# Kernel tuning notes

Hardware: AMD Instinct MI355X
Metric: run time of the kernel (lower is better)

Reference implementation:

```python
import jax, jax.numpy as jnp
import numpy as np

INPUT_DIM = 512
OUTPUT_DIM = 512
DEGREE = 7
ALPHA = 0.5


def setup_inputs() -> dict:
    key = jax.random.key(0)
    kx, kc = jax.random.split(key)
    x = jax.random.normal(kx, (8192, INPUT_DIM), dtype=jnp.float32)
    std = 1.0 / (INPUT_DIM * (DEGREE + 1))
    laguerre_coeffs = jax.random.normal(kc, (INPUT_DIM, OUTPUT_DIM, DEGREE + 1), dtype=jnp.float32) * std
    return {"x": x, "laguerre_coeffs": laguerre_coeffs}


def reference(x, laguerre_coeffs):
    # x: [B, I] -> tanh squashed
    xt = jnp.tanh(x.reshape(-1, INPUT_DIM))
    # Build Laguerre basis L_0..L_degree via the standard recurrence:
    # k*L_k = (2(k-1)+1+alpha - x)*L_{k-1} - (k-1+alpha)*L_{k-2}
    L0 = jnp.ones_like(xt)
    basis = [L0]
    if DEGREE > 0:
        L1 = 1.0 + ALPHA - xt
        basis.append(L1)
        Lkm2, Lkm1 = L0, L1
        for k in range(2, DEGREE + 1):
            Lk = ((2 * (k - 1) + 1 + ALPHA - xt) * Lkm1 - (k - 1 + ALPHA) * Lkm2) / k
            basis.append(Lk)
            Lkm2, Lkm1 = Lkm1, Lk
    laguerre = jnp.stack(basis, axis=-1)  # [B, I, D+1]
    y = jnp.einsum('bid,iod->bo', laguerre, laguerre_coeffs)
    return y
```

## Files before the change

kernel.cpp:

```cpp
#include <hip/hip_runtime.h>

#define B_ROWS 8192
#define IN_DIM 512
#define OUT_DIM 512
#define NDEG 8
#define KDIM (IN_DIM * NDEG)
#define ZSLICES 4
#define NKT 16
#define BM 256
#define BN 128
#define LDB 72

typedef short bf16x8 __attribute__((ext_vector_type(8)));
typedef float f32x4  __attribute__((ext_vector_type(4)));

__device__ __forceinline__ unsigned short f2bf(float f) {
  unsigned u = __float_as_uint(f);
  u += 0x7fffu + ((u >> 16) & 1u);
  return (unsigned short)(u >> 16);
}

__device__ __forceinline__ void laguerre8(float t, float* L) {
  L[0] = 1.0f;
  L[1] = 1.5f - t;
#pragma unroll
  for (int k = 2; k < NDEG; ++k)
    L[k] = ((2.0f * (float)k - 0.5f - t) * L[k - 1] -
            ((float)k - 0.5f) * L[k - 2]) * (1.0f / (float)k);
  }

__global__ void prep_kernel(const float* __restrict__ x, const float* __restrict__ cf,
                            unsigned short* __restrict__ A, unsigned short* __restrict__ Bt) {
  int g = blockIdx.x;
  if (g < (B_ROWS * IN_DIM) / 256) {
    int idx = g * 256 + threadIdx.x;
    int b = idx >> 9, i = idx & 511;
    float L[NDEG];
    laguerre8(tanhf(x[idx]), L);
    uint4 v;
    v.x = (unsigned)f2bf(L[0]) | ((unsigned)f2bf(L[1]) << 16);
    v.y = (unsigned)f2bf(L[2]) | ((unsigned)f2bf(L[3]) << 16);
    v.z = (unsigned)f2bf(L[4]) | ((unsigned)f2bf(L[5]) << 16);
    v.w = (unsigned)f2bf(L[6]) | ((unsigned)f2bf(L[7]) << 16);
    int T = b >> 8, r = b & 255, kt = i >> 3, c = i & 7;
    size_t chunk = ((size_t)(T * 64 + kt)) * 2048 + r * 8 + (c ^ (r & 7));
    ((uint4*)A)[chunk] = v;
  } else {
    int idx = (g - (B_ROWS * IN_DIM) / 256) * 256 + threadIdx.x;
    int i = idx >> 9, o = idx & 511;
    const float4* cp = (const float4*)(cf + (size_t)idx * 8);
    float4 c0 = cp[0], c1 = cp[1];
    uint4 v;
    v.x = (unsigned)f2bf(c0.x) | ((unsigned)f2bf(c0.y) << 16);
    v.y = (unsigned)f2bf(c0.z) | ((unsigned)f2bf(c0.w) << 16);
    v.z = (unsigned)f2bf(c1.x) | ((unsigned)f2bf(c1.y) << 16);
    v.w = (unsigned)f2bf(c1.z) | ((unsigned)f2bf(c1.w) << 16);
    ((uint4*)Bt)[o * 512 + i] = v;
  }
}

__global__ __launch_bounds__(512, 2) void gemm_kernel(const unsigned short* __restrict__ A,
                                                      const unsigned short* __restrict__ Bt,
                                                      unsigned short* __restrict__ P) {
  __shared__ unsigned short lds[51200];

  const int tid = threadIdx.x;
  const int lane = tid & 63;
  const int w = tid >> 6;
  const int wm = w >> 1, wn = w & 1;

  const int g = blockIdx.x;
  const int xcd = g & 7, idx = g >> 3;
  const int z = xcd >> 1;
  const int y = (xcd & 1) * 16 + (idx & 15);
  const int bn = (idx >> 4) * BN;

  const uint4* Ag = (const uint4*)A;
  const uint4* Bg = (const uint4*)Bt;
  const size_t tile0 = ((size_t)(y * 64 + z * NKT)) * 2048;

  const int rB = tid >> 2, cB = (tid & 3) * 2;

  const int arow = lane & 15, hi = lane >> 4;
  const int swz0 = hi ^ (arow & 7);
  const int aoff0 = (wm * 64 + arow) * 64 + swz0 * 8;
  const int aoff1 = (wm * 64 + arow) * 64 + (swz0 ^ 4) * 8;
  const int boff  = (wn * 64 + arow) * LDB;

  f32x4 zero = {0.f, 0.f, 0.f, 0.f};
  f32x4 acc[4][4];
#pragma unroll
  for (int mi = 0; mi < 4; ++mi)
#pragma unroll
    for (int ni = 0; ni < 4; ++ni) acc[mi][ni] = zero;

  uint4 rb0 = Bg[(size_t)(bn + rB) * 512 + z * NKT * 8 + cB];
  uint4 rb1 = Bg[(size_t)(bn + rB) * 512 + z * NKT * 8 + cB + 1];
  {
    size_t base = tile0 + w * 256;
    unsigned short* dst = lds + w * 2048;
#pragma unroll
    for (int j = 0; j < 4; ++j)
      __builtin_amdgcn_global_load_lds(
          (const __attribute__((address_space(1))) unsigned int*)(Ag + base + j * 64 + lane),
          (__attribute__((address_space(3))) unsigned int*)(dst + j * 512), 16, 0, 0);
  }
  *(uint4*)&lds[32768 + rB * LDB + cB * 8] = rb0;
  *(uint4*)&lds[32768 + rB * LDB + (cB + 1) * 8] = rb1;
  __syncthreads();

#pragma unroll 2
  for (int kt = 0; kt < NKT; ++kt) {
    const int cur = kt & 1, nb = cur ^ 1;
    if (kt + 1 < NKT) {
      rb0 = Bg[(size_t)(bn + rB) * 512 + (z * NKT + kt + 1) * 8 + cB];
      rb1 = Bg[(size_t)(bn + rB) * 512 + (z * NKT + kt + 1) * 8 + cB + 1];
      size_t base = tile0 + (size_t)(kt + 1) * 2048 + w * 256;
      unsigned short* dst = lds + nb * 16384 + w * 2048;
#pragma unroll
      for (int j = 0; j < 4; ++j)
        __builtin_amdgcn_global_load_lds(
            (const __attribute__((address_space(1))) unsigned int*)(Ag + base + (size_t)(kt + 1) * 0 + base - base + j * 64 + lane),
            (__attribute__((address_space(3))) unsigned int*)(dst + j * 512), 16, 0, 0);
      __builtin_amdgcn_sched_barrier(0);
    }

    const unsigned short* Ac = lds + cur * 16384;
    const unsigned short* Bc = lds + 32768 + cur * 9216;
    bf16x8 af0[4], af1[4], bf0[4], bf1[4];
#pragma unroll
    for (int mi = 0; mi < 4; ++mi) {
      af0[mi] = *(const bf16x8*)(Ac + aoff0 + mi * 1024);
      af1[mi] = *(const bf16x8*)(Ac + aoff1 + mi * 1024);
    }
#pragma unroll
    for (int ni = 0; ni < 4; ++ni) {
      bf0[ni] = *(const bf16x8*)(Bc + boff + ni * 16 * LDB + hi * 8);
      bf1[ni] = *(const bf16x8*)(Bc + boff + ni * 16 * LDB + 32 + hi * 8);
    }
    __builtin_amdgcn_s_setprio(1);
#pragma unroll
    for (int mi = 0; mi < 4; ++mi)
#pragma unroll
      for (int ni = 0; ni < 4; ++ni)
        acc[mi][ni] = __builtin_amdgcn_mfma_f32_16x16x32_bf16(af0[mi], bf0[ni], acc[mi][ni], 0, 0, 0);
#pragma unroll
    for (int mi = 0; mi < 4; ++mi)
#pragma unroll
      for (int ni = 0; ni < 4; ++ni)
        acc[mi][ni] = __builtin_amdgcn_mfma_f32_16x16x32_bf16(af1[mi], bf1[ni], acc[mi][ni], 0, 0, 0);
    __builtin_amdgcn_s_setprio(0);

    if (kt + 1 < NKT) {
      unsigned short* BsN = lds + 32768 + nb * 9216;
      *(uint4*)&BsN[rB * LDB + cB * 8] = rb0;
      *(uint4*)&BsN[rB * LDB + (cB + 1) * 8] = rb1;
    }
    __syncthreads();
  }

  unsigned short* W = lds + w * 4096;
#pragma unroll
  for (int mi = 0; mi < 4; ++mi)
#pragma unroll
    for (int ni = 0; ni < 4; ++ni) {
      int col = ni * 16 + arow;
      int c8 = col >> 3, cpos = col & 7;
#pragma unroll
      for (int r = 0; r < 4; ++r) {
        int row = mi * 16 + hi * 4 + r;
        W[row * 64 + ((c8 ^ (row & 7)) << 3) + cpos] = f2bf(acc[mi][ni][r]);
      }
    }
  const int rr = lane >> 3, cc = lane & 7;
#pragma unroll
  for (int it = 0; it < 8; ++it) {
    int row = it * 8 + rr;
    uint4 v = *(uint4*)&W[row * 64 + ((cc ^ (row & 7)) << 3)];
    size_t pr = ((size_t)z * B_ROWS + (y * 256 + wm * 64 + row)) * 512 + bn + wn * 64 + cc * 8;
    *(uint4*)&P[pr] = v;
  }
}

__global__ void reduce_kernel(const unsigned short* __restrict__ P, float* __restrict__ out) {
  size_t t = (size_t)blockIdx.x * 256 + threadIdx.x;
  const uint4* p = (const uint4*)P;
  const size_t stride = (size_t)B_ROWS * OUT_DIM / 8;
  float s[8] = {0, 0, 0, 0, 0, 0, 0, 0};
#pragma unroll
  for (int zz = 0; zz < ZSLICES; ++zz) {
    uint4 v = p[t + zz * stride];
    unsigned q[4] = {v.x, v.y, v.z, v.w};
#pragma unroll
    for (int j = 0; j < 4; ++j) {
      s[2 * j]     += __uint_as_float((q[j] & 0xffffu) << 16);
      s[2 * j + 1] += __uint_as_float(q[j] & 0xffff0000u);
    }
  }
  float4 o0 = {s[0], s[1], s[2], s[3]}, o1 = {s[4], s[5], s[6], s[7]};
  ((float4*)out)[t * 2]     = o0;
  ((float4*)out)[t * 2 + 1] = o1;
}

__global__ void naive_kernel(const float* __restrict__ x, const float* __restrict__ c,
                             float* __restrict__ out) {
  __shared__ float bas[IN_DIM * NDEG];
  int b = blockIdx.x;
  for (int i = threadIdx.x; i < IN_DIM; i += 256) {
    float t = tanhf(x[(size_t)b * IN_DIM + i]);
    float L[NDEG];
    laguerre8(t, L);
#pragma unroll
    for (int d = 0; d < NDEG; ++d) bas[i * NDEG + d] = L[d];
  }
  __syncthreads();
  for (int o = threadIdx.x; o < OUT_DIM; o += 256) {
    float acc = 0.f;
    for (int i = 0; i < IN_DIM; ++i) {
      const float* cp = c + ((size_t)i * OUT_DIM + o) * NDEG;
#pragma unroll
      for (int d = 0; d < NDEG; ++d) acc += bas[i * NDEG + d] * cp[d];
    }
    out[(size_t)b * OUT_DIM + o] = acc;
  }
}

extern "C" void kernel_launch(void* const* d_in, const int* in_sizes, int n_in,
                              void* d_out, int out_size, void* d_ws, size_t ws_size,
                              hipStream_t stream) {
  const float* x    = (const float*)d_in[0];
  const float* coef = (const float*)d_in[1];
  float* out = (float*)d_out;

  const size_t A_BYTES  = (size_t)B_ROWS * KDIM * 2;
  const size_t P_BYTES  = (size_t)ZSLICES * B_ROWS * OUT_DIM * 2;
  const size_t BT_BYTES = (size_t)OUT_DIM * KDIM * 2;

  if (ws_size >= A_BYTES + P_BYTES + BT_BYTES) {
    unsigned short* Abuf = (unsigned short*)d_ws;
    unsigned short* Pp   = (unsigned short*)((char*)d_ws + A_BYTES);
    unsigned short* Bt   = (unsigned short*)((char*)d_ws + A_BYTES + P_BYTES);
    prep_kernel<<<(B_ROWS * IN_DIM + IN_DIM * OUT_DIM) / 256, 256, 0, stream>>>(x, coef, Abuf, Bt);
    gemm_kernel<<<512, 512, 0, stream>>>(Abuf, Bt, Pp);
    reduce_kernel<<<(B_ROWS * OUT_DIM / 8) / 256, 256, 0, stream>>>(Pp, out);
  } else {
    naive_kernel<<<B_ROWS, 256, 0, stream>>>(x, coef, out);
  }
}
```

Measured before the change: 75.14 us.

## Enlarge GEMM tile to 256x256 with swizzled B layout and async LDS loads

```diff
diff --git a/kernel.cpp b/kernel.cpp
--- a/kernel.cpp
+++ b/kernel.cpp
@@ -7,9 +7,6 @@
 #define KDIM (IN_DIM * NDEG)
 #define ZSLICES 4
 #define NKT 16
-#define BM 256
-#define BN 128
-#define LDB 72
 
 typedef short bf16x8 __attribute__((ext_vector_type(8)));
 typedef float f32x4  __attribute__((ext_vector_type(4)));
@@ -27,7 +24,8 @@
   for (int k = 2; k < NDEG; ++k)
     L[k] = ((2.0f * (float)k - 0.5f - t) * L[k - 1] -
             ((float)k - 0.5f) * L[k - 2]) * (1.0f / (float)k);
-  }
+}
+
 
 __global__ void prep_kernel(const float* __restrict__ x, const float* __restrict__ cf,
                             unsigned short* __restrict__ A, unsigned short* __restrict__ Bt) {
@@ -42,8 +40,8 @@
     v.y = (unsigned)f2bf(L[2]) | ((unsigned)f2bf(L[3]) << 16);
     v.z = (unsigned)f2bf(L[4]) | ((unsigned)f2bf(L[5]) << 16);
     v.w = (unsigned)f2bf(L[6]) | ((unsigned)f2bf(L[7]) << 16);
-    int T = b >> 8, r = b & 255, kt = i >> 3, c = i & 7;
-    size_t chunk = ((size_t)(T * 64 + kt)) * 2048 + r * 8 + (c ^ (r & 7));
+    int h = b >> 7, rb = b & 127, t = i >> 3, c = i & 7;
+    size_t chunk = ((size_t)(h * 64 + t)) * 1024 + (rb >> 6) * 512 + (rb & 63) * 8 + (c ^ (rb & 7));
     ((uint4*)A)[chunk] = v;
   } else {
     int idx = (g - (B_ROWS * IN_DIM) / 256) * 256 + threadIdx.x;
@@ -55,113 +53,115 @@
     v.y = (unsigned)f2bf(c0.z) | ((unsigned)f2bf(c0.w) << 16);
     v.z = (unsigned)f2bf(c1.x) | ((unsigned)f2bf(c1.y) << 16);
     v.w = (unsigned)f2bf(c1.z) | ((unsigned)f2bf(c1.w) << 16);
-    ((uint4*)Bt)[o * 512 + i] = v;
+    int h = o >> 7, rb = o & 127, t = i >> 3, c = i & 7;
+    size_t chunk = ((size_t)(h * 64 + t)) * 1024 + (rb >> 6) * 512 + (rb & 63) * 8 + (c ^ (rb & 7));
+    ((uint4*)Bt)[chunk] = v;
   }
 }
 
 __global__ __launch_bounds__(512, 2) void gemm_kernel(const unsigned short* __restrict__ A,
                                                       const unsigned short* __restrict__ Bt,
                                                       unsigned short* __restrict__ P) {
-  __shared__ unsigned short lds[51200];
+  __shared__ unsigned short lds[65536];
 
   const int tid = threadIdx.x;
   const int lane = tid & 63;
   const int w = tid >> 6;
-  const int wm = w >> 1, wn = w & 1;
+  const int wm = w >> 2, wn = w & 3;
 
   const int g = blockIdx.x;
-  const int xcd = g & 7, idx = g >> 3;
-  const int z = xcd >> 1;
-  const int y = (xcd & 1) * 16 + (idx & 15);
-  const int bn = (idx >> 4) * BN;
+  const int j0 = g >> 3, xx = g & 7;
+  const int My = ((j0 >> 3) << 3) | xx;
+  const int n = (j0 >> 2) & 1;
+  const int z = j0 & 3;
 
   const uint4* Ag = (const uint4*)A;
   const uint4* Bg = (const uint4*)Bt;
-  const size_t tile0 = ((size_t)(y * 64 + z * NKT)) * 2048;
-
-  const int rB = tid >> 2, cB = (tid & 3) * 2;
 
   const int arow = lane & 15, hi = lane >> 4;
-  const int swz0 = hi ^ (arow & 7);
-  const int aoff0 = (wm * 64 + arow) * 64 + swz0 * 8;
-  const int aoff1 = (wm * 64 + arow) * 64 + (swz0 ^ 4) * 8;
-  const int boff  = (wn * 64 + arow) * LDB;
+  const int e0 = (hi ^ (arow & 7)) * 8;
 
   f32x4 zero = {0.f, 0.f, 0.f, 0.f};
-  f32x4 acc[4][4];
-#pragma unroll
-  for (int mi = 0; mi < 4; ++mi)
+  f32x4 acc[8][4];
+#pragma unroll
+  for (int mi = 0; mi < 8; ++mi)
 #pragma unroll
     for (int ni = 0; ni < 4; ++ni) acc[mi][ni] = zero;
 
-  uint4 rb0 = Bg[(size_t)(bn + rB) * 512 + z * NKT * 8 + cB];
-  uint4 rb1 = Bg[(size_t)(bn + rB) * 512 + z * NKT * 8 + cB + 1];
-  {
-    size_t base = tile0 + w * 256;
-    unsigned short* dst = lds + w * 2048;
-#pragma unroll
-    for (int j = 0; j < 4; ++j)
-      __builtin_amdgcn_global_load_lds(
-          (const __attribute__((address_space(1))) unsigned int*)(Ag + base + j * 64 + lane),
-          (__attribute__((address_space(3))) unsigned int*)(dst + j * 512), 16, 0, 0);
-  }
-  *(uint4*)&lds[32768 + rB * LDB + cB * 8] = rb0;
-  *(uint4*)&lds[32768 + rB * LDB + (cB + 1) * 8] = rb1;
+  auto STAGE = [&](int tile, int buf) {
+    const int tg = z * NKT + tile;
+    const size_t cA0 = ((size_t)((My * 2 + 0) * 64 + tg)) * 1024 + w * 64 + lane;
+    const size_t cA1 = ((size_t)((My * 2 + 1) * 64 + tg)) * 1024 + w * 64 + lane;
+    const size_t cB0 = ((size_t)((n * 2 + 0) * 64 + tg)) * 1024 + w * 64 + lane;
+    const size_t cB1 = ((size_t)((n * 2 + 1) * 64 + tg)) * 1024 + w * 64 + lane;
+    unsigned short* dA = lds + buf * 16384 + w * 512;
+    unsigned short* dB = lds + 32768 + buf * 16384 + w * 512;
+#pragma unroll
+    for (int j = 0; j < 2; ++j) {
+      __builtin_amdgcn_global_load_lds(
+          (const __attribute__((address_space(1))) unsigned int*)(Ag + cA0 + j * 512),
+          (__attribute__((address_space(3))) unsigned int*)(dA + j * 4096), 16, 0, 0);
+      __builtin_amdgcn_global_load_lds(
+          (const __attribute__((address_space(1))) unsigned int*)(Ag + cA1 + j * 512),
+          (__attribute__((address_space(3))) unsigned int*)(dA + 8192 + j * 4096), 16, 0, 0);
+      __builtin_amdgcn_global_load_lds(
+          (const __attribute__((address_space(1))) unsigned int*)(Bg + cB0 + j * 512),
+          (__attribute__((address_space(3))) unsigned int*)(dB + j * 4096), 16, 0, 0);
+      __builtin_amdgcn_global_load_lds(
+          (const __attribute__((address_space(1))) unsigned int*)(Bg + cB1 + j * 512),
+          (__attribute__((address_space(3))) unsigned int*)(dB + 8192 + j * 4096), 16, 0, 0);
+    }
+  };
+
+  auto COMPUTE = [&](int buf) {
+    const unsigned short* Ab = lds + buf * 16384 + wm * 8192;
+    const unsigned short* Bb = lds + 32768 + buf * 16384 + (wn >> 1) * 8192 + (wn & 1) * 4096;
+#pragma unroll
+    for (int ks = 0; ks < 2; ++ks) {
+      bf16x8 af[8], bfr[4];
+#pragma unroll
+      for (int mi = 0; mi < 8; ++mi)
+        af[mi] = *(const bf16x8*)(Ab + (mi >> 2) * 4096 + ((mi & 3) * 16 + arow) * 64 + (e0 ^ (ks * 32)));
+#pragma unroll
+      for (int ni = 0; ni < 4; ++ni)
+        bfr[ni] = *(const bf16x8*)(Bb + (ni * 16 + arow) * 64 + (e0 ^ (ks * 32)));
+      __builtin_amdgcn_s_setprio(1);
+#pragma unroll
+      for (int mi = 0; mi < 8; ++mi)
+#pragma unroll
+        for (int ni = 0; ni < 4; ++ni)
+          acc[mi][ni] = __builtin_amdgcn_mfma_f32_16x16x32_bf16(af[mi], bfr[ni], acc[mi][ni], 0, 0, 0);
+      __builtin_amdgcn_s_setprio(0);
+    }
+  };
+
+  STAGE(0, 0);
+  STAGE(1, 1);
+  asm volatile("s_waitcnt vmcnt(8)" ::: "memory");
+  __builtin_amdgcn_sched_barrier(0);
+  __builtin_amdgcn_s_barrier();
+
+  for (int t = 0; t < NKT - 2; ++t) {
+    const int cur = t & 1;
+    COMPUTE(cur);
+    asm volatile("s_waitcnt lgkmcnt(0)" ::: "memory");
+    __builtin_amdgcn_sched_barrier(0);
+    __builtin_amdgcn_s_barrier();
+    STAGE(t + 2, cur);
+    asm volatile("s_waitcnt vmcnt(8)" ::: "memory");
+    __builtin_amdgcn_sched_barrier(0);
+    __builtin_amdgcn_s_barrier();
+  }
+  COMPUTE(0);
+  asm volatile("s_waitcnt vmcnt(0)" ::: "memory");
+  __builtin_amdgcn_sched_barrier(0);
+  __builtin_amdgcn_s_barrier();
+  COMPUTE(1);
   __syncthreads();
 
-#pragma unroll 2
-  for (int kt = 0; kt < NKT; ++kt) {
-    const int cur = kt & 1, nb = cur ^ 1;
-    if (kt + 1 < NKT) {
-      rb0 = Bg[(size_t)(bn + rB) * 512 + (z * NKT + kt + 1) * 8 + cB];
-      rb1 = Bg[(size_t)(bn + rB) * 512 + (z * NKT + kt + 1) * 8 + cB + 1];
-      size_t base = tile0 + (size_t)(kt + 1) * 2048 + w * 256;
-      unsigned short* dst = lds + nb * 16384 + w * 2048;
-#pragma unroll
-      for (int j = 0; j < 4; ++j)
-        __builtin_amdgcn_global_load_lds(
-            (const __attribute__((address_space(1))) unsigned int*)(Ag + base + (size_t)(kt + 1) * 0 + base - base + j * 64 + lane),
-            (__attribute__((address_space(3))) unsigned int*)(dst + j * 512), 16, 0, 0);
-      __builtin_amdgcn_sched_barrier(0);
-    }
-
-    const unsigned short* Ac = lds + cur * 16384;
-    const unsigned short* Bc = lds + 32768 + cur * 9216;
-    bf16x8 af0[4], af1[4], bf0[4], bf1[4];
-#pragma unroll
-    for (int mi = 0; mi < 4; ++mi) {
-      af0[mi] = *(const bf16x8*)(Ac + aoff0 + mi * 1024);
-      af1[mi] = *(const bf16x8*)(Ac + aoff1 + mi * 1024);
-    }
-#pragma unroll
-    for (int ni = 0; ni < 4; ++ni) {
-      bf0[ni] = *(const bf16x8*)(Bc + boff + ni * 16 * LDB + hi * 8);
-      bf1[ni] = *(const bf16x8*)(Bc + boff + ni * 16 * LDB + 32 + hi * 8);
-    }
-    __builtin_amdgcn_s_setprio(1);
-#pragma unroll
-    for (int mi = 0; mi < 4; ++mi)
-#pragma unroll
-      for (int ni = 0; ni < 4; ++ni)
-        acc[mi][ni] = __builtin_amdgcn_mfma_f32_16x16x32_bf16(af0[mi], bf0[ni], acc[mi][ni], 0, 0, 0);
-#pragma unroll
-    for (int mi = 0; mi < 4; ++mi)
-#pragma unroll
-      for (int ni = 0; ni < 4; ++ni)
-        acc[mi][ni] = __builtin_amdgcn_mfma_f32_16x16x32_bf16(af1[mi], bf1[ni], acc[mi][ni], 0, 0, 0);
-    __builtin_amdgcn_s_setprio(0);
-
-    if (kt + 1 < NKT) {
-      unsigned short* BsN = lds + 32768 + nb * 9216;
-      *(uint4*)&BsN[rB * LDB + cB * 8] = rb0;
-      *(uint4*)&BsN[rB * LDB + (cB + 1) * 8] = rb1;
-    }
-    __syncthreads();
-  }
-
-  unsigned short* W = lds + w * 4096;
-#pragma unroll
-  for (int mi = 0; mi < 4; ++mi)
+  unsigned short* W = lds + w * 8192;
+#pragma unroll
+  for (int mi = 0; mi < 8; ++mi)
 #pragma unroll
     for (int ni = 0; ni < 4; ++ni) {
       int col = ni * 16 + arow;
@@ -174,10 +174,10 @@
     }
   const int rr = lane >> 3, cc = lane & 7;
 #pragma unroll
-  for (int it = 0; it < 8; ++it) {
+  for (int it = 0; it < 16; ++it) {
     int row = it * 8 + rr;
     uint4 v = *(uint4*)&W[row * 64 + ((cc ^ (row & 7)) << 3)];
-    size_t pr = ((size_t)z * B_ROWS + (y * 256 + wm * 64 + row)) * 512 + bn + wn * 64 + cc * 8;
+    size_t pr = ((size_t)z * B_ROWS + My * 256 + wm * 128 + row) * 512 + n * 256 + wn * 64 + cc * 8;
     *(uint4*)&P[pr] = v;
   }
 }
@@ -241,7 +241,7 @@
     unsigned short* Pp   = (unsigned short*)((char*)d_ws + A_BYTES);
     unsigned short* Bt   = (unsigned short*)((char*)d_ws + A_BYTES + P_BYTES);
     prep_kernel<<<(B_ROWS * IN_DIM + IN_DIM * OUT_DIM) / 256, 256, 0, stream>>>(x, coef, Abuf, Bt);
-    gemm_kernel<<<512, 512, 0, stream>>>(Abuf, Bt, Pp);
+    gemm_kernel<<<256, 512, 0, stream>>>(Abuf, Bt, Pp);
     reduce_kernel<<<(B_ROWS * OUT_DIM / 8) / 256, 256, 0, stream>>>(Pp, out);
   } else {
     naive_kernel<<<B_ROWS, 256, 0, stream>>>(x, coef, out);
```

Measured after the change: 67.95 us. 9.6% less time.
